# Kernel tuning notes

Measured on AMD Instinct MI355X. Metric: run time of the kernel, lower is better.

## Reference

```python
import jax, jax.numpy as jnp
import numpy as np
import math

B, T, D, H = 4, 2048, 1024, 8
DK = D // H


def _rel_shift(x):
    # x: [B, H, T, P] with P = 2T-1 (Transformer-XL relative shift)
    b, h, q, p = x.shape
    x = jnp.pad(x, ((0, 0), (0, 0), (0, 0), (1, 0)))
    x = x.reshape(b, h, p + 1, q)[:, :, 1:]
    return x.reshape(b, h, q, p)


def setup_inputs() -> dict:
    key = jax.random.key(0)
    ks = jax.random.split(key, 9)
    s = 0.02
    x = jax.random.normal(ks[0], (B, T, D), jnp.float32)
    pos_emb = jax.random.normal(ks[1], (1, 2 * T - 1, D), jnp.float32)
    Wq = jax.random.normal(ks[2], (D, D), jnp.float32) * s
    Wk = jax.random.normal(ks[3], (D, D), jnp.float32) * s
    Wv = jax.random.normal(ks[4], (D, D), jnp.float32) * s
    Wo = jax.random.normal(ks[5], (D, D), jnp.float32) * s
    Wp = jax.random.normal(ks[6], (D, D), jnp.float32) * s
    pos_bias_u = jax.random.normal(ks[7], (H, DK), jnp.float32) * s
    pos_bias_v = jax.random.normal(ks[8], (H, DK), jnp.float32) * s
    return {"x": x, "pos_emb": pos_emb, "Wq": Wq, "Wk": Wk, "Wv": Wv,
            "Wo": Wo, "Wp": Wp, "pos_bias_u": pos_bias_u, "pos_bias_v": pos_bias_v}


def reference(x, pos_emb, Wq, Wk, Wv, Wo, Wp, pos_bias_u, pos_bias_v):
    b, t, d = x.shape
    h, dk = pos_bias_u.shape
    inv_sdk = 1.0 / math.sqrt(dk)
    # projections (torch Linear: y = x @ W.T)
    q = (x @ Wq.T).reshape(b, t, h, dk)          # [B,T,H,DK]
    k = (x @ Wk.T).reshape(b, t, h, dk)          # [B,T,H,DK]
    v = (x @ Wv.T).reshape(b, t, h, dk)          # [B,T,H,DK]
    p = (pos_emb @ Wp.T).reshape(-1, h, dk)      # [P,H,DK], P = 2T-1
    # content and position scores
    matrix_ac = jnp.einsum('bqhd,bkhd->bhqk', q + pos_bias_u, k)   # [B,H,T,T]
    matrix_bd = jnp.einsum('bqhd,phd->bhqp', q + pos_bias_v, p)    # [B,H,T,2T-1]
    matrix_bd = _rel_shift(matrix_bd)[..., :t]                     # [B,H,T,T]
    scores = (matrix_ac + matrix_bd) * inv_sdk
    attn = jax.nn.softmax(scores, axis=-1)
    out = jnp.einsum('bhqk,bkhd->bqhd', attn, v).reshape(b, t, h * dk)
    return out @ Wo.T
```

## Files before the change

kernel.cpp:

```cpp
#include <hip/hip_runtime.h>
#include <cstdint>
#include <math.h>

#define B_   4
#define T_   2048
#define D_   1024
#define H_   8
#define DK_  128
#define P_   4095
#define PS_  4096

typedef unsigned short ushort_t;
typedef __attribute__((ext_vector_type(8))) short short8;
typedef __attribute__((ext_vector_type(4))) float floatx4;

__device__ inline float bf2f(ushort_t s) {
    return __uint_as_float(((unsigned int)s) << 16);
}
__device__ inline ushort_t f2bf(float f) {
    unsigned int u = __float_as_uint(f);
    u += 0x7fffu + ((u >> 16) & 1u);
    return (ushort_t)(u >> 16);
}

__device__ inline floatx4 mfma16(short8 a, short8 b, floatx4 c) {
    return __builtin_amdgcn_mfma_f32_16x16x32_bf16(a, b, c, 0, 0, 0);
}

__device__ inline void gload_lds16(const ushort_t* g, ushort_t* l) {
    __builtin_amdgcn_global_load_lds(
        (const __attribute__((address_space(1))) unsigned int*)g,
        (__attribute__((address_space(3))) unsigned int*)l, 16, 0, 0);
}

__global__ void detect_kernel(const ushort_t* x, int* flag) {
    if (blockIdx.x == 0 && threadIdx.x == 0) {
        int m = 0;
        for (int i = 0; i < 64; ++i) {
            float v = bf2f(x[2 * i]);
            float a = fabsf(v);
            if (!(a == 0.0f || (a > 1e-20f && a < 1e10f))) m = 1;
        }
        flag[0] = m;
    }
}

#define CV_TOT 17826816
template <int MODE>
__global__ __launch_bounds__(256) void convert_kernel(
    const int* __restrict__ flag,
    const void* __restrict__ x, const void* __restrict__ pe,
    const void* __restrict__ wq, const void* __restrict__ wk,
    const void* __restrict__ wv, const void* __restrict__ wo,
    const void* __restrict__ wp, const void* __restrict__ ub,
    const void* __restrict__ vb, ushort_t* __restrict__ dst)
{
    if (flag[0] != MODE) return;
    const size_t i = ((size_t)blockIdx.x * 256 + threadIdx.x) * 4;
    if (i >= CV_TOT) return;
    const void* s; size_t off;
    if (i < 8388608)       { s = x;  off = i; }
    else if (i < 12581888) { s = pe; off = i - 8388608; }
    else if (i < 13630464) { s = wq; off = i - 12581888; }
    else if (i < 14679040) { s = wk; off = i - 13630464; }
    else if (i < 15727616) { s = wv; off = i - 14679040; }
    else if (i < 16776192) { s = wo; off = i - 15727616; }
    else if (i < 17824768) { s = wp; off = i - 16776192; }
    else if (i < 17825792) { s = ub; off = i - 17824768; }
    else                   { s = vb; off = i - 17825792; }
    const size_t d = i + (i >= 12581888 ? 1024 : 0);
    if (MODE == 0) {
        *(uint2*)(dst + d) = *(const uint2*)((const ushort_t*)s + off);
    } else {
        float4 f = *(const float4*)((const float*)s + off);
        uint2 o;
        o.x = (unsigned)f2bf(f.x) | ((unsigned)f2bf(f.y) << 16);
        o.y = (unsigned)f2bf(f.z) | ((unsigned)f2bf(f.w) << 16);
        *(uint2*)(dst + d) = o;
    }
}

__global__ __launch_bounds__(256, 3) void gemm_mfma(
    const int* __restrict__ flag,
    const ushort_t* __restrict__ A, const ushort_t* __restrict__ W,
    void* __restrict__ C, int smode)
{
    if (smode == 3 && flag[0] != 0) return;
    if (smode == 4 && flag[0] != 1) return;
    const int K = 1024, N = 1024;

    __shared__ ushort_t Al[16 * 512];
    __shared__ ushort_t Wl[16 * 512];

    const int tid  = threadIdx.x;
    const int w    = tid >> 6, lane = tid & 63;
    const int r15  = lane & 15, quad = lane >> 4;
    const int wm   = w >> 1, wn = w & 1;
    const int m0   = blockIdx.y * 128, n0 = blockIdx.x * 128;

    floatx4 acc[4][4];
    const floatx4 z4 = {0.f, 0.f, 0.f, 0.f};
#pragma unroll
    for (int mt = 0; mt < 4; ++mt)
#pragma unroll
        for (int nt = 0; nt < 4; ++nt) acc[mt][nt] = z4;

    for (int k0 = 0; k0 < K; k0 += 64) {
#pragma unroll
        for (int ss = 0; ss < 4; ++ss) {
            const int s  = w * 4 + ss;
            const int mg = s >> 1, ks = s & 1;
            const int row = mg * 16 + r15;
            const int col = k0 + ks * 32 + quad * 8;
            gload_lds16(A + (size_t)(m0 + row) * K + col, &Al[s * 512]);
            gload_lds16(W + (size_t)(n0 + row) * K + col, &Wl[s * 512]);
        }
        __syncthreads();

        short8 af[2][4], bf[2][4];
#pragma unroll
        for (int ks = 0; ks < 2; ++ks) {
#pragma unroll
            for (int mt = 0; mt < 4; ++mt)
                af[ks][mt] = *(const short8*)&Al[(((wm * 4 + mt) * 2 + ks) * 64 + lane) * 8];
#pragma unroll
            for (int nt = 0; nt < 4; ++nt)
                bf[ks][nt] = *(const short8*)&Wl[(((wn * 4 + nt) * 2 + ks) * 64 + lane) * 8];
        }
#pragma unroll
        for (int ks = 0; ks < 2; ++ks)
#pragma unroll
            for (int mt = 0; mt < 4; ++mt)
#pragma unroll
                for (int nt = 0; nt < 4; ++nt)
                    acc[mt][nt] = mfma16(af[ks][mt], bf[ks][nt], acc[mt][nt]);
        __syncthreads();
    }

#pragma unroll
    for (int mt = 0; mt < 4; ++mt)
#pragma unroll
        for (int nt = 0; nt < 4; ++nt)
#pragma unroll
            for (int i = 0; i < 4; ++i) {
                const int m = m0 + wm * 64 + mt * 16 + quad * 4 + i;
                const int n = n0 + wn * 64 + nt * 16 + r15;
                const float v = acc[mt][nt][i];
                if (smode == 0) {
                    const int b = m >> 11, t = m & (T_ - 1);
                    const int h = n >> 7, dk = n & (DK_ - 1);
                    ((ushort_t*)C)[(((size_t)(b * H_ + h)) * T_ + t) * DK_ + dk] = f2bf(v);
                } else if (smode == 1) {
                    const int h = n >> 7, dk = n & (DK_ - 1);
                    ((ushort_t*)C)[((size_t)h * PS_ + m) * DK_ + dk] = f2bf(v);
                } else if (smode == 2) {
                    const int b = m >> 11, t = m & (T_ - 1);
                    const int h = n >> 7, dk = n & (DK_ - 1);
                    ((ushort_t*)C)[((size_t)(b * H_ + h) * DK_ + dk) * T_ + t] = f2bf(v);
                } else if (smode == 3) {
                    ((ushort_t*)C)[(size_t)m * N + n] = f2bf(v);
                } else {
                    ((float*)C)[(size_t)m * N + n] = v;
                }
            }
}

__global__ __launch_bounds__(256, 2) void attn_mfma(
    const ushort_t* __restrict__ qg,
    const ushort_t* __restrict__ kgl,
    const ushort_t* __restrict__ vt,
    const ushort_t* __restrict__ pg,
    const ushort_t* __restrict__ ubb,
    const ushort_t* __restrict__ vbb,
    ushort_t* __restrict__ ao)
{
    __shared__ ushort_t K_lds[16 * 512];
    __shared__ ushort_t V_lds[16 * 512];
    __shared__ ushort_t P_lds[32 * 512];
    __shared__ __align__(16) ushort_t pr_lds[4][1024];

    const int tid  = threadIdx.x;
    const int w    = tid >> 6;
    const int lane = tid & 63;
    const int r15  = lane & 15;
    const int quad = lane >> 4;
    const int bh   = blockIdx.y;
    const int h    = bh & (H_ - 1);
    const int b    = bh >> 3;
    const int q0b  = blockIdx.x * 64;
    const int q0w  = q0b + w * 16;

    short8 quA[4], qvA[4];
    {
        const ushort_t* qrow = qg + ((size_t)bh * T_ + q0w + r15) * DK_;
#pragma unroll
        for (int ks = 0; ks < 4; ++ks) {
            const int dk0 = ks * 32 + quad * 8;
            uint4 q4 = *(const uint4*)(qrow + dk0);
            uint4 u4 = *(const uint4*)(ubb + (size_t)h * DK_ + dk0);
            uint4 v4 = *(const uint4*)(vbb + (size_t)h * DK_ + dk0);
            const ushort_t* qs = (const ushort_t*)&q4;
            const ushort_t* us = (const ushort_t*)&u4;
            const ushort_t* vs = (const ushort_t*)&v4;
#pragma unroll
            for (int j = 0; j < 8; ++j) {
                const float qf = bf2f(qs[j]);
                quA[ks][j] = (short)f2bf(qf + bf2f(us[j]));
                qvA[ks][j] = (short)f2bf(qf + bf2f(vs[j]));
            }
        }
    }

    int src[4], hi[4];
#pragma unroll
    for (int i = 0; i < 4; ++i) {
        const int c = r15 + 15 - quad * 4 - i;
        src[i] = quad * 16 + (c & 15);
        hi[i]  = c >> 4;
    }

    floatx4 o[8];
    const floatx4 z4 = {0.f, 0.f, 0.f, 0.f};
#pragma unroll
    for (int g = 0; g < 8; ++g) o[g] = z4;
    float mrun[4], lrun[4];
#pragma unroll
    for (int i = 0; i < 4; ++i) { mrun[i] = -1e30f; lrun[i] = 0.f; }

    const float scale = 0.08838834764831845f;

    for (int kc0 = 0; kc0 < T_; kc0 += 64) {
        const int pbb = kc0 - q0b + 1984;

#pragma unroll
        for (int ss = 0; ss < 4; ++ss) {
            const int ck = w * 4 + ss;
            gload_lds16(kgl + ((size_t)bh * T_ + kc0 + w * 16 + r15) * DK_ + ss * 32 + quad * 8,
                        &K_lds[ck * 512]);
            const int cv = w * 4 + ss;
            const int og = cv >> 1, ks2 = cv & 1;
            gload_lds16(vt + ((size_t)(bh * DK_ + og * 16 + r15)) * T_ + kc0 + ks2 * 32 + quad * 8,
                        &V_lds[cv * 512]);
        }
#pragma unroll
        for (int ss = 0; ss < 8; ++ss) {
            const int cp = w * 8 + ss;
            const int gb = cp >> 2, ks = cp & 3;
            gload_lds16(pg + ((size_t)h * PS_ + pbb + gb * 16 + r15) * DK_ + ks * 32 + quad * 8,
                        &P_lds[cp * 512]);
        }
        __syncthreads();

        floatx4 ac[4];
#pragma unroll
        for (int g = 0; g < 4; ++g) {
            ac[g] = z4;
#pragma unroll
            for (int ks = 0; ks < 4; ++ks)
                ac[g] = mfma16(quA[ks],
                               *(const short8*)&K_lds[((g * 4 + ks) * 64 + lane) * 8],
                               ac[g]);
        }
        floatx4 bd[5];
#pragma unroll
        for (int g = 0; g < 5; ++g) {
            bd[g] = z4;
            const int gb = (3 - w) + g;
#pragma unroll
            for (int ks = 0; ks < 4; ++ks)
                bd[g] = mfma16(qvA[ks],
                               *(const short8*)&P_lds[((gb * 4 + ks) * 64 + lane) * 8],
                               bd[g]);
        }

        float pr[4][4];
        float mc[4], alpha[4];
#pragma unroll
        for (int i = 0; i < 4; ++i) {
            float mm = -1e30f;
#pragma unroll
            for (int g = 0; g < 4; ++g) {
                const float lo = __shfl(bd[g][i],     src[i], 64);
                const float hh = __shfl(bd[g + 1][i], src[i], 64);
                const float s  = (ac[g][i] + (hi[i] ? hh : lo)) * scale;
                pr[g][i] = s;
                mm = fmaxf(mm, s);
            }
            mc[i] = mm;
        }
#pragma unroll
        for (int i = 0; i < 4; ++i) {
#pragma unroll
            for (int mk = 1; mk < 16; mk <<= 1)
                mc[i] = fmaxf(mc[i], __shfl_xor(mc[i], mk));
            const float mn = fmaxf(mrun[i], mc[i]);
            alpha[i] = __expf(mrun[i] - mn);
            mrun[i] = mn;
            float ls = 0.f;
#pragma unroll
            for (int g = 0; g < 4; ++g) {
                const float e = __expf(pr[g][i] - mn);
                pr[g][i] = e;
                ls += e;
            }
#pragma unroll
            for (int mk = 1; mk < 16; mk <<= 1)
                ls += __shfl_xor(ls, mk);
            lrun[i] = lrun[i] * alpha[i] + ls;
        }
#pragma unroll
        for (int g = 0; g < 8; ++g)
#pragma unroll
            for (int i = 0; i < 4; ++i) o[g][i] *= alpha[i];

#pragma unroll
        for (int g = 0; g < 4; ++g) {
            const int unit = (g >> 1) * 4 + (g & 1) * 2 + (r15 >> 3);
#pragma unroll
            for (int i = 0; i < 4; ++i)
                pr_lds[w][(unit * 16 + quad * 4 + i) * 8 + (r15 & 7)] = f2bf(pr[g][i]);
        }
        short8 pa[2];
#pragma unroll
        for (int ks2 = 0; ks2 < 2; ++ks2)
            pa[ks2] = *(const short8*)&pr_lds[w][(ks2 * 64 + lane) * 8];

#pragma unroll
        for (int og = 0; og < 8; ++og)
#pragma unroll
            for (int ks2 = 0; ks2 < 2; ++ks2)
                o[og] = mfma16(pa[ks2],
                               *(const short8*)&V_lds[((og * 2 + ks2) * 64 + lane) * 8],
                               o[og]);
        __syncthreads();
    }

    float inv[4];
#pragma unroll
    for (int i = 0; i < 4; ++i) inv[i] = 1.0f / lrun[i];
#pragma unroll
    for (int og = 0; og < 8; ++og)
#pragma unroll
        for (int i = 0; i < 4; ++i) {
            const size_t idx =
                ((size_t)(b * T_ + q0w + quad * 4 + i)) * D_ + h * DK_ + og * 16 + r15;
            ao[idx] = f2bf(o[og][i] * inv[i]);
        }
}

extern "C" void kernel_launch(void* const* d_in, const int* in_sizes, int n_in,
                              void* d_out, int out_size, void* d_ws, size_t ws_size,
                              hipStream_t stream) {
    const void* x  = d_in[0];
    const void* pe = d_in[1];
    const void* Wq = d_in[2];
    const void* Wk = d_in[3];
    const void* Wv = d_in[4];
    const void* Wo = d_in[5];
    const void* Wp = d_in[6];
    const void* ub = d_in[7];
    const void* vb = d_in[8];

    int* flag = (int*)d_ws;
    ushort_t* arena = (ushort_t*)d_ws + 16;
    ushort_t* xb   = arena;
    ushort_t* peb  = arena + 8388608;
    ushort_t* wqb  = arena + 12582912;
    ushort_t* wkb  = wqb + 1048576;
    ushort_t* wvb  = wkb + 1048576;
    ushort_t* wob  = wvb + 1048576;
    ushort_t* wpb  = wob + 1048576;
    ushort_t* ubb  = arena + 17825792;
    ushort_t* vbb  = ubb + 1024;
    ushort_t* q_ws  = arena + 17827840;
    ushort_t* k_ws  = q_ws + 8388608;
    ushort_t* vt_ws = k_ws + 8388608;
    ushort_t* p_ws  = vt_ws + 8388608;
    ushort_t* ao_ws = xb;

    detect_kernel<<<1, 64, 0, stream>>>((const ushort_t*)x, flag);

    const int cvb = CV_TOT / 4 / 256;
    convert_kernel<0><<<cvb, 256, 0, stream>>>(flag, x, pe, Wq, Wk, Wv, Wo, Wp, ub, vb, arena);
    convert_kernel<1><<<cvb, 256, 0, stream>>>(flag, x, pe, Wq, Wk, Wv, Wo, Wp, ub, vb, arena);

    const dim3 gX(8, 64);
    const dim3 gP(8, 32);
    gemm_mfma<<<gX, 256, 0, stream>>>(flag, xb,  wqb, q_ws, 0);
    gemm_mfma<<<gX, 256, 0, stream>>>(flag, xb,  wkb, k_ws, 0);
    gemm_mfma<<<gX, 256, 0, stream>>>(flag, xb,  wvb, vt_ws, 2);
    gemm_mfma<<<gP, 256, 0, stream>>>(flag, peb, wpb, p_ws, 1);

    attn_mfma<<<dim3(T_ / 64, B_ * H_), 256, 0, stream>>>(
        q_ws, k_ws, vt_ws, p_ws, ubb, vbb, ao_ws);

    gemm_mfma<<<gX, 256, 0, stream>>>(flag, ao_ws, wob, d_out, 3);
    gemm_mfma<<<gX, 256, 0, stream>>>(flag, ao_ws, wob, d_out, 4);
}
```

Baseline: 588.3 us.

## Use DPP row-max, lazy rescaling, and MFMA row-sum in flash softmax loop

Replaces the shuffle-based 16-lane max reduction with DPP row operations. The output and denominator are rescaled only when some row's running max increases. The per-row exp sum is computed by two extra MFMAs against a vector of bf16 ones, which removes the shuffle-based sum reduction. This cuts cross-lane shuffle traffic and VALU work in the attention inner loop. In exchange, the denominator is now summed from bf16-rounded probabilities and the loop gains a wave-uniform branch.

```diff
diff --git a/kernel.cpp b/kernel.cpp
--- a/kernel.cpp
+++ b/kernel.cpp
@@ -31,6 +31,19 @@
     __builtin_amdgcn_global_load_lds(
         (const __attribute__((address_space(1))) unsigned int*)g,
         (__attribute__((address_space(3))) unsigned int*)l, 16, 0, 0);
+}
+
+__device__ inline float rowmax16(float x) {
+    int t;
+    t = __builtin_amdgcn_update_dpp(0, __float_as_int(x), 0x128, 0xf, 0xf, true);
+    x = fmaxf(x, __int_as_float(t));
+    t = __builtin_amdgcn_update_dpp(0, __float_as_int(x), 0x124, 0xf, 0xf, true);
+    x = fmaxf(x, __int_as_float(t));
+    t = __builtin_amdgcn_update_dpp(0, __float_as_int(x), 0x4E, 0xf, 0xf, true);
+    x = fmaxf(x, __int_as_float(t));
+    t = __builtin_amdgcn_update_dpp(0, __float_as_int(x), 0xB1, 0xf, 0xf, true);
+    x = fmaxf(x, __int_as_float(t));
+    return x;
 }
 
 __global__ void detect_kernel(const ushort_t* x, int* flag) {
@@ -223,9 +236,14 @@
     const floatx4 z4 = {0.f, 0.f, 0.f, 0.f};
 #pragma unroll
     for (int g = 0; g < 8; ++g) o[g] = z4;
-    float mrun[4], lrun[4];
-#pragma unroll
-    for (int i = 0; i < 4; ++i) { mrun[i] = -1e30f; lrun[i] = 0.f; }
+    floatx4 lacc = z4;
+    float mrun[4];
+#pragma unroll
+    for (int i = 0; i < 4; ++i) mrun[i] = -1e30f;
+
+    short8 ones8;
+#pragma unroll
+    for (int j = 0; j < 8; ++j) ones8[j] = (short)0x3F80;
 
     const float scale = 0.08838834764831845f;
 
@@ -274,7 +292,7 @@
         }
 
         float pr[4][4];
-        float mc[4], alpha[4];
+        float mc[4];
 #pragma unroll
         for (int i = 0; i < 4; ++i) {
             float mm = -1e30f;
@@ -286,32 +304,30 @@
                 pr[g][i] = s;
                 mm = fmaxf(mm, s);
             }
-            mc[i] = mm;
-        }
-#pragma unroll
-        for (int i = 0; i < 4; ++i) {
-#pragma unroll
-            for (int mk = 1; mk < 16; mk <<= 1)
-                mc[i] = fmaxf(mc[i], __shfl_xor(mc[i], mk));
-            const float mn = fmaxf(mrun[i], mc[i]);
-            alpha[i] = __expf(mrun[i] - mn);
-            mrun[i] = mn;
-            float ls = 0.f;
-#pragma unroll
-            for (int g = 0; g < 4; ++g) {
-                const float e = __expf(pr[g][i] - mn);
-                pr[g][i] = e;
-                ls += e;
+            mc[i] = rowmax16(mm);
+        }
+        const bool nd = (mc[0] > mrun[0]) | (mc[1] > mrun[1]) |
+                        (mc[2] > mrun[2]) | (mc[3] > mrun[3]);
+        if (__any(nd)) {
+            float alpha[4];
+#pragma unroll
+            for (int i = 0; i < 4; ++i) {
+                const float mn = fmaxf(mrun[i], mc[i]);
+                alpha[i] = __expf(mrun[i] - mn);
+                mrun[i] = mn;
             }
 #pragma unroll
-            for (int mk = 1; mk < 16; mk <<= 1)
-                ls += __shfl_xor(ls, mk);
-            lrun[i] = lrun[i] * alpha[i] + ls;
-        }
-#pragma unroll
-        for (int g = 0; g < 8; ++g)
-#pragma unroll
-            for (int i = 0; i < 4; ++i) o[g][i] *= alpha[i];
+            for (int g = 0; g < 8; ++g)
+#pragma unroll
+                for (int i = 0; i < 4; ++i) o[g][i] *= alpha[i];
+#pragma unroll
+            for (int i = 0; i < 4; ++i) lacc[i] *= alpha[i];
+        }
+#pragma unroll
+        for (int g = 0; g < 4; ++g)
+#pragma unroll
+            for (int i = 0; i < 4; ++i)
+                pr[g][i] = __expf(pr[g][i] - mrun[i]);
 
 #pragma unroll
         for (int g = 0; g < 4; ++g) {
@@ -332,12 +348,14 @@
                 o[og] = mfma16(pa[ks2],
                                *(const short8*)&V_lds[((og * 2 + ks2) * 64 + lane) * 8],
                                o[og]);
+        lacc = mfma16(pa[0], ones8, lacc);
+        lacc = mfma16(pa[1], ones8, lacc);
         __syncthreads();
     }
 
     float inv[4];
 #pragma unroll
-    for (int i = 0; i < 4; ++i) inv[i] = 1.0f / lrun[i];
+    for (int i = 0; i < 4; ++i) inv[i] = 1.0f / lacc[i];
 #pragma unroll
     for (int og = 0; og < 8; ++og)
 #pragma unroll
```

After: 596.8 us. About the same (+1.4%).
